# Performance work log

Hardware: AMD Instinct MI355X
Metric: run time of the kernel (lower is better)

The kernel has to match this reference:

```python
import jax, jax.numpy as jnp
import numpy as np

B, D, H, L = 4096, 8192, 4096, 128


def binarize_ste(v, thresh):
    # BinarizeTensorThresh with straight-through gradient (identity backward)
    return v + jax.lax.stop_gradient((v > thresh).astype(v.dtype) - v)


def setup_inputs() -> dict:
    key = jax.random.key(0)
    k0, k1, k2, k3 = jax.random.split(key, 4)
    x = (jax.random.uniform(k0, (B, D), jnp.float32) < 0.1).astype(jnp.float32)  # sparse binary data
    enc_weight = jax.random.normal(k1, (H, D), jnp.float32) * (2.0 / (H + D)) ** 0.5 + 0.5  # xavier-ish around binarize thresh
    bias0 = -jax.random.uniform(k2, (H,), jnp.float32)  # clipBias keeps bias <= 0
    bias3 = jnp.zeros((D,), jnp.float32)  # act3.noBias()
    clf_weight = jax.random.uniform(k3, (L, H), jnp.float32)  # clamped to [0,1]
    return {"x": x, "enc_weight": enc_weight, "bias0": bias0, "bias3": bias3, "clf_weight": clf_weight}


def reference(x, enc_weight, bias0, bias3, clf_weight):
    wb = binarize_ste(enc_weight, 0.5)                 # [H, D] binarized encoder weights
    h = jnp.einsum('bd,hd->bh', x, wb)                 # fc0_enc
    z = binarize_ste(h + bias0, 1.0)                   # act0: BinaryActivation (STE threshold)
    classification = jnp.einsum('bh,lh->bl', z, clf_weight)  # classifier (no bias)
    recon = jnp.einsum('bh,hd->bd', z, wb)             # fc3_dec: tied transposed binarized weights
    output = binarize_ste(recon + bias3, 1.0)          # act3
    return output, classification, z
```

## Files before the change

### kernel.cpp

```cpp
#include <hip/hip_runtime.h>
#include <cstdint>

typedef unsigned long long u64;

constexpr int B = 4096;
constexpr int D = 8192;
constexpr int H = 4096;
constexpr int L = 128;
constexpr int DW = D / 64;
constexpr int HW = H / 64;

__global__ __launch_bounds__(256) void k_A(const float* __restrict__ x,
                                           const float* __restrict__ e,
                                           const float* __restrict__ bias0,
                                           const float* __restrict__ clf,
                                           u64* __restrict__ xp,
                                           u64* __restrict__ wbpw,
                                           int* __restrict__ cmin,
                                           float* __restrict__ R) {
    __shared__ float s[256];
    int r = blockIdx.x;
    int lane = threadIdx.x & 63;
    int wave = threadIdx.x >> 6;

    if (r < B + H) {
        bool is_x = (r < B);
        const float* row = is_x ? (x + (size_t)r * D) : (e + (size_t)(r - B) * D);
        #pragma unroll
        for (int it = 0; it < 8; ++it) {
            int chunk = wave * 8 + it;
            int base = chunk * 256;
            u64 m[4];
            #pragma unroll
            for (int k = 0; k < 4; ++k) {
                float v = row[base + k * 64 + lane];
                m[k] = __ballot(v > 0.5f);
            }
            if (lane == 0) {
                if (is_x) {
                    u64* orow = xp + (size_t)r * DW + chunk * 4;
                    orow[0] = m[0]; orow[1] = m[1]; orow[2] = m[2]; orow[3] = m[3];
                } else {
                    int h = r - B;
                    #pragma unroll
                    for (int k = 0; k < 4; ++k)
                        wbpw[(size_t)(chunk * 4 + k) * H + h] = m[k];
                }
            }
        }
    } else if (r < B + H + 16) {
        int h = (r - B - H) * 256 + threadIdx.x;
        float b0 = bias0[h];
        int c = (int)(1.0f - b0);
        if (c < 0) c = 0;
        int guard = 0;
        while ((float)c + b0 <= 1.0f && guard++ < 100000) ++c;
        while (c > 0 && (float)(c - 1) + b0 > 1.0f) --c;
        cmin[h] = c;
    } else {
        int l = r - (B + H + 16);
        float acc = 0.f;
        for (int h = threadIdx.x; h < H; h += 256) acc += clf[(size_t)l * H + h];
        s[threadIdx.x] = acc;
        __syncthreads();
        for (int off = 128; off > 0; off >>= 1) {
            if ((int)threadIdx.x < off) s[threadIdx.x] += s[threadIdx.x + off];
            __syncthreads();
        }
        if (threadIdx.x == 0) R[l] = s[0];
    }
}

__global__ __launch_bounds__(256) void k_B(const u64* __restrict__ wbpw,
                                           const float* __restrict__ bias3,
                                           float* __restrict__ basef) {
    int w = blockIdx.x;
    int lane = threadIdx.x & 63;
    int wave = threadIdx.x >> 6;
    __shared__ int sc[4][64];
    int cnt = 0;
    #pragma unroll 1
    for (int g = wave; g < 64; g += 4) {
        u64 W = wbpw[(size_t)w * H + g * 64 + lane];
        #pragma unroll 1
        for (int jj = 0; jj < 64; ++jj) {
            u64 m = __ballot((int)((W >> jj) & 1ull));
            if (lane == jj) cnt += (int)__popcll(m);
        }
    }
    sc[wave][lane] = cnt;
    __syncthreads();
    if (wave == 0) {
        int tot = sc[0][lane] + sc[1][lane] + sc[2][lane] + sc[3][lane];
        int d = w * 64 + lane;
        basef[d] = ((float)tot + bias3[d] > 1.0f) ? 1.0f : 0.0f;
    }
}

__global__ __launch_bounds__(256) void k_Z(const u64* __restrict__ xp,
                                           const u64* __restrict__ wbpw,
                                           const int* __restrict__ cmin,
                                           const float* __restrict__ basef,
                                           const float* __restrict__ R,
                                           const float* __restrict__ clf,
                                           const float* __restrict__ bias3,
                                           float* __restrict__ out0,
                                           float* __restrict__ out1,
                                           float* __restrict__ zout) {
    __shared__ u64 sxw[DW];
    __shared__ u64 zrow[HW];
    __shared__ int s_nz;
    int b = blockIdx.x;
    int lane = threadIdx.x & 63;
    int wave = threadIdx.x >> 6;

    if (threadIdx.x < DW) sxw[threadIdx.x] = xp[(size_t)b * DW + threadIdx.x];
    __syncthreads();
    u64 x0 = sxw[0], x1 = sxw[1], x2 = sxw[2], x3 = sxw[3];

    #pragma unroll 1
    for (int i = 0; i < HW / 4; ++i) {
        int hb = wave * (HW / 4) + i;
        int h = hb * 64 + lane;
        int cm = cmin[h];
        const u64* __restrict__ wp = wbpw + hb * 64 + lane;
        u64 w0 = wp[0];
        u64 w1 = wp[(size_t)H];
        u64 w2 = wp[(size_t)2 * H];
        u64 w3 = wp[(size_t)3 * H];
        int cnt = (int)__popcll(x0 & w0) + (int)__popcll(x1 & w1)
                + (int)__popcll(x2 & w2) + (int)__popcll(x3 & w3);
        if (!__all(cnt >= cm)) {
            #pragma unroll 1
            for (int w = 4; w < DW; ++w) {
                if (cnt < cm) cnt += (int)__popcll(sxw[w] & wp[(size_t)w * H]);
                if (__all(cnt >= cm)) break;
            }
        }
        int zb = (cnt >= cm) ? 1 : 0;
        u64 m = __ballot(zb);
        if (lane == 0) zrow[hb] = m;
    }
    __syncthreads();

    if (wave == 0) {
        int c = (int)__popcll(zrow[lane]);
        #pragma unroll
        for (int off = 32; off > 0; off >>= 1) c += __shfl_down(c, off);
        if (lane == 0) s_nz = H - c;
    }
    __syncthreads();
    int nz = s_nz;

    {
        float* zr = zout + (size_t)b * H;
        #pragma unroll
        for (int k = 0; k < 4; ++k) {
            int t = threadIdx.x + k * 256;
            u64 wzd = zrow[t >> 4];
            int j0 = (t & 15) * 4;
            float4 f;
            f.x = ((wzd >> (j0 + 0)) & 1ull) ? 1.0f : 0.0f;
            f.y = ((wzd >> (j0 + 1)) & 1ull) ? 1.0f : 0.0f;
            f.z = ((wzd >> (j0 + 2)) & 1ull) ? 1.0f : 0.0f;
            f.w = ((wzd >> (j0 + 3)) & 1ull) ? 1.0f : 0.0f;
            ((float4*)zr)[t] = f;
        }
    }

    if (nz == 0) {
        if (threadIdx.x < L) out1[(size_t)b * L + threadIdx.x] = R[threadIdx.x];
        float4* o4 = (float4*)(out0 + (size_t)b * D);
        const float4* b4 = (const float4*)basef;
        #pragma unroll
        for (int k = 0; k < 8; ++k) {
            int t = threadIdx.x + k * 256;
            o4[t] = b4[t];
        }
    } else {
        if (threadIdx.x < L) {
            int l = threadIdx.x;
            float acc = 0.f;
            for (int wh = 0; wh < HW; ++wh) {
                u64 m = zrow[wh];
                while (m) {
                    int j = __ffsll(m) - 1;
                    acc += clf[(size_t)l * H + wh * 64 + j];
                    m &= m - 1;
                }
            }
            out1[(size_t)b * L + l] = acc;
        }
        for (int w = wave; w < DW; w += 4) {
            int acc = 0;
            for (int hb = 0; hb < HW; ++hb) {
                u64 Wj = wbpw[(size_t)w * H + hb * 64 + lane];
                u64 zm = zrow[hb];
                u64 masked = ((zm >> lane) & 1ull) ? Wj : 0ull;
                for (int jj = 0; jj < 64; ++jj) {
                    u64 bal = __ballot((int)((masked >> jj) & 1ull));
                    if (lane == jj) acc += (int)__popcll(bal);
                }
            }
            int d = w * 64 + lane;
            out0[(size_t)b * D + d] = ((float)acc + bias3[d] > 1.0f) ? 1.0f : 0.0f;
        }
    }
}


extern "C" void kernel_launch(void* const* d_in, const int* in_sizes, int n_in,
                              void* d_out, int out_size, void* d_ws, size_t ws_size,
                              hipStream_t stream) {
    const float* x   = (const float*)d_in[0];
    const float* ew  = (const float*)d_in[1];
    const float* b0  = (const float*)d_in[2];
    const float* b3  = (const float*)d_in[3];
    const float* clf = (const float*)d_in[4];

    float* out0 = (float*)d_out;
    float* out1 = out0 + (size_t)B * D;
    float* zout = out1 + (size_t)B * L;

    char* ws = (char*)d_ws;
    u64* xp      = (u64*)(ws);
    u64* wbpw    = (u64*)(ws + (4ull << 20));
    float* basef = (float*)(ws + (8ull << 20));
    float* R     = (float*)(ws + (8ull << 20) + 32768);
    int* cmin    = (int*)(ws + (8ull << 20) + 32768 + 512);

    k_A<<<B + H + 16 + L, 256, 0, stream>>>(x, ew, b0, clf, xp, wbpw, cmin, R);
    k_B<<<DW, 256, 0, stream>>>(wbpw, b3, basef);
    k_Z<<<B, 256, 0, stream>>>(xp, wbpw, cmin, basef, R, clf, b3,
                               out0, out1, zout);
}
```

Baseline: 468.0 us.

## Fuse x bit-packing into main kernel and repack weight binarization

Bit-packing of x moves out of the prep kernel and into the main per-row kernel, which reads the float row with float4 loads and packs bytes into shared memory, so the packed-x workspace round trip goes away. Weight packing becomes its own kernel using vectorized loads and shared-memory byte packing instead of per-lane ballots. The column-count, cmin and clf row-sum work are merged into one small second kernel. The cost is that the main kernel now reads the full x row of 32KB per block before it can start its own work.

New measurement: 456.6 us. -2.4%, faster.

```diff
diff --git a/kernel.cpp b/kernel.cpp
--- a/kernel.cpp
+++ b/kernel.cpp
@@ -10,46 +10,61 @@
 constexpr int DW = D / 64;
 constexpr int HW = H / 64;
 
-__global__ __launch_bounds__(256) void k_A(const float* __restrict__ x,
-                                           const float* __restrict__ e,
+__global__ __launch_bounds__(256) void k_P(const float* __restrict__ e,
+                                           u64* __restrict__ wbpw) {
+    __shared__ u64 sw[DW];
+    unsigned char* sb = (unsigned char*)sw;
+    int h = blockIdx.x;
+    const float4* row4 = (const float4*)(e + (size_t)h * D);
+    #pragma unroll
+    for (int j = 0; j < 4; ++j) {
+        int t = j * 256 + threadIdx.x;
+        float4 a = row4[2 * t];
+        float4 c = row4[2 * t + 1];
+        unsigned v = (a.x > 0.5f ? 1u : 0u) | (a.y > 0.5f ? 2u : 0u)
+                   | (a.z > 0.5f ? 4u : 0u) | (a.w > 0.5f ? 8u : 0u)
+                   | (c.x > 0.5f ? 16u : 0u) | (c.y > 0.5f ? 32u : 0u)
+                   | (c.z > 0.5f ? 64u : 0u) | (c.w > 0.5f ? 128u : 0u);
+        sb[t] = (unsigned char)v;
+    }
+    __syncthreads();
+    if (threadIdx.x < DW)
+        wbpw[(size_t)threadIdx.x * H + h] = sw[threadIdx.x];
+}
+
+__global__ __launch_bounds__(256) void k_B(const u64* __restrict__ wbpw,
                                            const float* __restrict__ bias0,
+                                           const float* __restrict__ bias3,
                                            const float* __restrict__ clf,
-                                           u64* __restrict__ xp,
-                                           u64* __restrict__ wbpw,
+                                           float* __restrict__ basef,
                                            int* __restrict__ cmin,
                                            float* __restrict__ R) {
+    __shared__ int sc[4][64];
     __shared__ float s[256];
     int r = blockIdx.x;
     int lane = threadIdx.x & 63;
     int wave = threadIdx.x >> 6;
-
-    if (r < B + H) {
-        bool is_x = (r < B);
-        const float* row = is_x ? (x + (size_t)r * D) : (e + (size_t)(r - B) * D);
-        #pragma unroll
-        for (int it = 0; it < 8; ++it) {
-            int chunk = wave * 8 + it;
-            int base = chunk * 256;
-            u64 m[4];
-            #pragma unroll
-            for (int k = 0; k < 4; ++k) {
-                float v = row[base + k * 64 + lane];
-                m[k] = __ballot(v > 0.5f);
-            }
-            if (lane == 0) {
-                if (is_x) {
-                    u64* orow = xp + (size_t)r * DW + chunk * 4;
-                    orow[0] = m[0]; orow[1] = m[1]; orow[2] = m[2]; orow[3] = m[3];
-                } else {
-                    int h = r - B;
-                    #pragma unroll
-                    for (int k = 0; k < 4; ++k)
-                        wbpw[(size_t)(chunk * 4 + k) * H + h] = m[k];
-                }
-            }
-        }
-    } else if (r < B + H + 16) {
-        int h = (r - B - H) * 256 + threadIdx.x;
+    if (r < DW) {
+        int w = r;
+        int cnt = 0;
+        #pragma unroll 1
+        for (int g = wave; g < 64; g += 4) {
+            u64 W = wbpw[(size_t)w * H + g * 64 + lane];
+            #pragma unroll 1
+            for (int jj = 0; jj < 64; ++jj) {
+                u64 m = __ballot((int)((W >> jj) & 1ull));
+                if (lane == jj) cnt += (int)__popcll(m);
+            }
+        }
+        sc[wave][lane] = cnt;
+        __syncthreads();
+        if (wave == 0) {
+            int tot = sc[0][lane] + sc[1][lane] + sc[2][lane] + sc[3][lane];
+            int d = w * 64 + lane;
+            basef[d] = ((float)tot + bias3[d] > 1.0f) ? 1.0f : 0.0f;
+        }
+    } else if (r < DW + 16) {
+        int h = (r - DW) * 256 + threadIdx.x;
         float b0 = bias0[h];
         int c = (int)(1.0f - b0);
         if (c < 0) c = 0;
@@ -58,9 +73,9 @@
         while (c > 0 && (float)(c - 1) + b0 > 1.0f) --c;
         cmin[h] = c;
     } else {
-        int l = r - (B + H + 16);
+        int l = r - (DW + 16);
         float acc = 0.f;
-        for (int h = threadIdx.x; h < H; h += 256) acc += clf[(size_t)l * H + h];
+        for (int hh = threadIdx.x; hh < H; hh += 256) acc += clf[(size_t)l * H + hh];
         s[threadIdx.x] = acc;
         __syncthreads();
         for (int off = 128; off > 0; off >>= 1) {
@@ -71,33 +86,7 @@
     }
 }
 
-__global__ __launch_bounds__(256) void k_B(const u64* __restrict__ wbpw,
-                                           const float* __restrict__ bias3,
-                                           float* __restrict__ basef) {
-    int w = blockIdx.x;
-    int lane = threadIdx.x & 63;
-    int wave = threadIdx.x >> 6;
-    __shared__ int sc[4][64];
-    int cnt = 0;
-    #pragma unroll 1
-    for (int g = wave; g < 64; g += 4) {
-        u64 W = wbpw[(size_t)w * H + g * 64 + lane];
-        #pragma unroll 1
-        for (int jj = 0; jj < 64; ++jj) {
-            u64 m = __ballot((int)((W >> jj) & 1ull));
-            if (lane == jj) cnt += (int)__popcll(m);
-        }
-    }
-    sc[wave][lane] = cnt;
-    __syncthreads();
-    if (wave == 0) {
-        int tot = sc[0][lane] + sc[1][lane] + sc[2][lane] + sc[3][lane];
-        int d = w * 64 + lane;
-        basef[d] = ((float)tot + bias3[d] > 1.0f) ? 1.0f : 0.0f;
-    }
-}
-
-__global__ __launch_bounds__(256) void k_Z(const u64* __restrict__ xp,
+__global__ __launch_bounds__(256) void k_Z(const float* __restrict__ x,
                                            const u64* __restrict__ wbpw,
                                            const int* __restrict__ cmin,
                                            const float* __restrict__ basef,
@@ -110,11 +99,23 @@
     __shared__ u64 sxw[DW];
     __shared__ u64 zrow[HW];
     __shared__ int s_nz;
+    unsigned char* sxb = (unsigned char*)sxw;
     int b = blockIdx.x;
     int lane = threadIdx.x & 63;
     int wave = threadIdx.x >> 6;
 
-    if (threadIdx.x < DW) sxw[threadIdx.x] = xp[(size_t)b * DW + threadIdx.x];
+    const float4* xr4 = (const float4*)(x + (size_t)b * D);
+    #pragma unroll
+    for (int j = 0; j < 4; ++j) {
+        int t = j * 256 + threadIdx.x;
+        float4 a = xr4[2 * t];
+        float4 c = xr4[2 * t + 1];
+        unsigned v = (a.x > 0.5f ? 1u : 0u) | (a.y > 0.5f ? 2u : 0u)
+                   | (a.z > 0.5f ? 4u : 0u) | (a.w > 0.5f ? 8u : 0u)
+                   | (c.x > 0.5f ? 16u : 0u) | (c.y > 0.5f ? 32u : 0u)
+                   | (c.z > 0.5f ? 64u : 0u) | (c.w > 0.5f ? 128u : 0u);
+        sxb[t] = (unsigned char)v;
+    }
     __syncthreads();
     u64 x0 = sxw[0], x1 = sxw[1], x2 = sxw[2], x3 = sxw[3];
 
@@ -223,14 +224,13 @@
     float* zout = out1 + (size_t)B * L;
 
     char* ws = (char*)d_ws;
-    u64* xp      = (u64*)(ws);
-    u64* wbpw    = (u64*)(ws + (4ull << 20));
-    float* basef = (float*)(ws + (8ull << 20));
-    float* R     = (float*)(ws + (8ull << 20) + 32768);
-    int* cmin    = (int*)(ws + (8ull << 20) + 32768 + 512);
-
-    k_A<<<B + H + 16 + L, 256, 0, stream>>>(x, ew, b0, clf, xp, wbpw, cmin, R);
-    k_B<<<DW, 256, 0, stream>>>(wbpw, b3, basef);
-    k_Z<<<B, 256, 0, stream>>>(xp, wbpw, cmin, basef, R, clf, b3,
+    u64* wbpw    = (u64*)(ws);
+    float* basef = (float*)(ws + (4ull << 20));
+    float* R     = (float*)(ws + (4ull << 20) + 32768);
+    int* cmin    = (int*)(ws + (4ull << 20) + 32768 + 512);
+
+    k_P<<<H, 256, 0, stream>>>(ew, wbpw);
+    k_B<<<DW + 16 + L, 256, 0, stream>>>(wbpw, b0, b3, clf, basef, cmin, R);
+    k_Z<<<B, 256, 0, stream>>>(x, wbpw, cmin, basef, R, clf, b3,
                                out0, out1, zout);
 }
```
